# Kernel optimization log

Hardware: AMD Instinct MI355X
Metric: run time of the kernel (lower is better)

Reference implementation:

```python
import jax, jax.numpy as jnp
from jax import lax
import numpy as np

N, C_IN, C_OUT, H, W, D = 16, 32, 64, 128, 128, 5


def setup_inputs() -> dict:
    key = jax.random.key(0)
    k1, k2, k3, k4 = jax.random.split(key, 4)
    x = jax.random.normal(k1, (N, 1, C_IN, H, W), jnp.float32)
    d = jax.random.normal(k2, (N, C_OUT, C_IN, D, D), jnp.float32)
    y = jax.random.normal(k3, (N, C_OUT, 1, H, W), jnp.float32)
    alpha = jax.random.uniform(k4, (N, 1, 1, 1), jnp.float32)
    return {"x": x, "d": d, "y": y, "alpha": alpha, "reg": 1.0}


def _cross_corr(wts, img, pad):
    # out[i, j, u, v] = sum_{h,w} wts[i,h,w] * img[j, h+u-pad, w+v-pad]
    # (valid sums, zero padding). Implements the per-sample full-image conv3d
    # of the torch code (cross-correlation, no kernel flip).
    out = lax.conv_general_dilated(img[:, None], wts[:, None], (1, 1),
                                   [(pad, pad), (pad, pad)])
    return out.transpose(1, 0, 2, 3)  # (Ci_wts, Cj_img, 2*pad+1, 2*pad+1)


def reference(x, d, y, alpha, reg):
    n, _, c_in, h, w = x.shape
    c_out, ds = d.shape[1], d.shape[-1]
    K = c_in * ds * ds
    # Full autocorrelation R[n,c0,c1,a,b] = sum x[c0,h,w]*x[c1,h+a-(ds-1), w+b-(ds-1)]
    R = jax.vmap(lambda xn: _cross_corr(xn, xn, ds - 1))(x[:, 0])  # (n,C,C,2ds-1,2ds-1)
    # Toeplitz block assembly: Q[(c0,p,q),(c1,s,t)] = R[c0,c1, s-p+ds-1, t-q+ds-1]
    shift = jnp.arange(ds)[None, :] - jnp.arange(ds)[:, None] + (ds - 1)  # [p,s]
    Qa = R[:, :, :, shift, :]            # (n,c0,c1,p,s,2ds-1)
    Qb = Qa[..., shift]                  # (n,c0,c1,p,s,q,t)
    Q = Qb.transpose(0, 1, 3, 5, 2, 4, 6).reshape(n, K, K)
    # X^T y: S[n,o,c,u,v] = sum y[o,h,w]*x[c, h+u-p0, w+v-p0], p0=(ds-1)//2
    S = jax.vmap(lambda yn, xn: _cross_corr(yn, xn, (ds - 1) // 2))(y[:, :, 0], x[:, 0])
    P = S.transpose(0, 2, 3, 4, 1).reshape(n, K, c_out)
    # Tikhonov regularization around previous dictionary d
    a = alpha.reshape(n, 1) * (h * w * reg / (ds * ds * c_in))  # (n,1)
    Q = Q + a[:, :, None] * jnp.eye(K, dtype=Q.dtype)
    P = P + a[:, :, None] * d.reshape(n, c_out, K).transpose(0, 2, 1)
    # Batched Cholesky solve: D = Q^{-1} P
    L = jnp.linalg.cholesky(Q)
    z = lax.linalg.triangular_solve(L, P, left_side=True, lower=True)
    Dsol = lax.linalg.triangular_solve(L, z, left_side=True, lower=True, transpose_a=True)
    return Dsol.reshape(n, c_in, ds, ds, c_out).transpose(0, 4, 1, 2, 3)
```

## Files before the change

kernel.cpp:

```cpp
#include <hip/hip_runtime.h>

#define R_SZ    737280
#define Q_SZ    10240000
#define P_SZ    819200
#define LI_SZ   1024000
#define W_SZ    4608000

typedef unsigned short u16;
typedef __attribute__((ext_vector_type(8))) short bf16x8;
typedef __attribute__((ext_vector_type(4))) float f32x4;

#define MFMA16(a, b, c) __builtin_amdgcn_mfma_f32_16x16x32_bf16(a, b, c, 0, 0, 0)

__device__ __forceinline__ float alpha_scale(const float* alpha, const float* reg, int n) {
  return alpha[n] * (16384.0f * reg[0] / 800.0f);
}

__device__ __forceinline__ u16 f2bf(float f) {
  union { float f; unsigned u; } v; v.f = f;
  unsigned r = v.u + 0x7FFFu + ((v.u >> 16) & 1u);
  return (u16)(r >> 16);
}
__device__ __forceinline__ float bf2f(u16 h) {
  union { unsigned u; float f; } v; v.u = ((unsigned)h) << 16; return v.f;
}

__device__ __forceinline__ bf16x8 load8(const u16* p) {
  union { uint4 d; bf16x8 v; } u;
  u.d = *(const uint4*)p;
  return u.v;
}

__device__ __forceinline__ bf16x8 build_frag(const unsigned* w, int s) {
  union { unsigned u[4]; bf16x8 v; } f;
  int b = s >> 1;
  if (s & 1) {
    #pragma unroll
    for (int k = 0; k < 4; ++k) f.u[k] = (w[b + k] >> 16) | (w[b + k + 1] << 16);
  } else {
    #pragma unroll
    for (int k = 0; k < 4; ++k) f.u[k] = w[b + k];
  }
  return f.v;
}

__device__ __forceinline__ void stage_row(u16* slot, int partStride,
                                          const float* __restrict__ img,
                                          int C, int r, bool valid,
                                          int tid, int nthr) {
  for (int idx = tid; idx < C * 16; idx += nthr) {
    int c = idx >> 4, m = idx & 15;
    float v[8];
    if (valid) {
      const float* p = img + ((size_t)c * 128 + r) * 128 + m * 8;
      float4 a = *(const float4*)p;
      float4 b = *(const float4*)(p + 4);
      v[0]=a.x; v[1]=a.y; v[2]=a.z; v[3]=a.w; v[4]=b.x; v[5]=b.y; v[6]=b.z; v[7]=b.w;
    } else {
      #pragma unroll
      for (int k = 0; k < 8; ++k) v[k] = 0.0f;
    }
    union { u16 s[8]; uint2 d[2]; } hh, ll;
    #pragma unroll
    for (int k = 0; k < 8; ++k) {
      u16 h = f2bf(v[k]);
      hh.s[k] = h;
      ll.s[k] = f2bf(v[k] - bf2f(h));
    }
    u16* dh = slot + c * 136 + 4 + m * 8;
    *(uint2*)(dh)     = hh.d[0];
    *(uint2*)(dh + 4) = hh.d[1];
    u16* dl = dh + partStride;
    *(uint2*)(dl)     = ll.d[0];
    *(uint2*)(dl + 4) = ll.d[1];
  }
}

#define SLOT_US 8704
#define PSTR_32 4352
#define YPSTR   8704

__global__ __launch_bounds__(640) void k_corrR_mfma(const float* __restrict__ x,
                                                    float* __restrict__ Rpart) {
  __shared__ __align__(16) u16 lds[5 * SLOT_US];
  int n  = blockIdx.x >> 4;
  int r0 = (blockIdx.x & 15) << 3;
  int tid = threadIdx.x;
  const float* xn = x + (size_t)n * 32 * 128 * 128;

  if (tid < 320) {
    int s = tid / 64, p = (tid >> 5) & 1, c = tid & 31;
    u16* b = lds + s * SLOT_US + p * PSTR_32 + c * 136;
    uint2 z; z.x = 0; z.y = 0;
    *(uint2*)b = z;
    *(uint2*)(b + 132) = z;
  }
  for (int rr = 0; rr < 5; ++rr) {
    int r = r0 + rr;
    stage_row(lds + (r % 5) * SLOT_US, PSTR_32, xn, 32, r, r < 128, tid, 640);
  }

  int wave = tid >> 6, lane = tid & 63;
  int du = wave >> 1, nt = wave & 1;
  int lm = lane & 15, q = lane >> 4;

  f32x4 acc[9][2];
  #pragma unroll
  for (int dvi = 0; dvi < 9; ++dvi)
    #pragma unroll
    for (int mt = 0; mt < 2; ++mt) acc[dvi][mt] = (f32x4){0.f, 0.f, 0.f, 0.f};

  for (int i = r0; i < r0 + 8; ++i) {
    __syncthreads();
    const u16* A  = lds + (i % 5) * SLOT_US;
    const u16* Bp = lds + ((i + du) % 5) * SLOT_US;
    #pragma unroll
    for (int ks = 0; ks < 4; ++ks) {
      int kb = ks * 32 + q * 8;
      bf16x8 af[2][2];
      #pragma unroll
      for (int pa = 0; pa < 2; ++pa)
        #pragma unroll
        for (int mt = 0; mt < 2; ++mt)
          af[pa][mt] = load8(A + pa * PSTR_32 + (mt * 16 + lm) * 136 + 4 + kb);
      #pragma unroll
      for (int pb = 0; pb < 2; ++pb) {
        const u16* wp = Bp + pb * PSTR_32 + (nt * 16 + lm) * 136 + kb;
        uint4 w0 = *(const uint4*)wp;
        uint4 w1 = *(const uint4*)(wp + 8);
        unsigned w[8] = {w0.x, w0.y, w0.z, w0.w, w1.x, w1.y, w1.z, w1.w};
        #pragma unroll
        for (int dvi = 0; dvi < 9; ++dvi) {
          bf16x8 bf = build_frag(w, dvi);
          #pragma unroll
          for (int mt = 0; mt < 2; ++mt)
            #pragma unroll
            for (int pa = 0; pa < 2; ++pa) {
              if (pa == 1 && pb == 1) continue;
              acc[dvi][mt] = MFMA16(af[pa][mt], bf, acc[dvi][mt]);
            }
        }
      }
    }
    __syncthreads();
    if (i + 1 < r0 + 8) {
      int r = i + 5;
      stage_row(lds + (r % 5) * SLOT_US, PSTR_32, xn, 32, r, r < 128, tid, 640);
    }
  }

  float* Rp = Rpart + (size_t)blockIdx.x * 46080;
  #pragma unroll
  for (int dvi = 0; dvi < 9; ++dvi)
    #pragma unroll
    for (int mt = 0; mt < 2; ++mt) {
      float* dst = Rp + (du * 9 + dvi) * 1024 + (nt * 16 + lm) * 32 + mt * 16 + q * 4;
      *(f32x4*)dst = acc[dvi][mt];
    }
}

__global__ void k_reduceR(const float* __restrict__ part, float* __restrict__ R) {
  int idx = blockIdx.x * 256 + threadIdx.x;
  int n = idx / 46080, rem = idx % 46080;
  const float* p = part + (size_t)n * 16 * 46080 + rem;
  float s = 0.0f;
  #pragma unroll
  for (int c = 0; c < 16; ++c) s += p[(size_t)c * 46080];
  R[idx] = s;
}

__global__ __launch_bounds__(640) void k_corrP_mfma(const float* __restrict__ x,
                                                    const float* __restrict__ y,
                                                    float* __restrict__ Ppart) {
  __shared__ __align__(16) u16 xs[5 * SLOT_US];
  __shared__ __align__(16) u16 ys[2 * YPSTR];
  int n  = blockIdx.x >> 4;
  int r0 = (blockIdx.x & 15) << 3;
  int tid = threadIdx.x;
  const float* xn = x + (size_t)n * 32 * 128 * 128;
  const float* yn = y + (size_t)n * 64 * 128 * 128;

  if (tid < 320) {
    int s = tid / 64, p = (tid >> 5) & 1, c = tid & 31;
    u16* b = xs + s * SLOT_US + p * PSTR_32 + c * 136;
    uint2 z; z.x = 0; z.y = 0;
    *(uint2*)b = z;
    *(uint2*)(b + 132) = z;
  }
  for (int rr = -2; rr <= 2; ++rr) {
    int r = r0 + rr;
    stage_row(xs + ((r + 10) % 5) * SLOT_US, PSTR_32, xn, 32, r,
              (r >= 0 && r < 128), tid, 640);
  }
  stage_row(ys, YPSTR, yn, 64, r0, true, tid, 640);

  int wave = tid >> 6, lane = tid & 63;
  int du = (wave >> 1) - 2, mh = wave & 1;
  int lm = lane & 15, q = lane >> 4;

  f32x4 acc[5][2][2];
  #pragma unroll
  for (int dvi = 0; dvi < 5; ++dvi)
    #pragma unroll
    for (int mt = 0; mt < 2; ++mt)
      #pragma unroll
      for (int nt = 0; nt < 2; ++nt)
        acc[dvi][mt][nt] = (f32x4){0.f, 0.f, 0.f, 0.f};

  for (int i = r0; i < r0 + 8; ++i) {
    __syncthreads();
    const u16* Bp = xs + ((i + du + 10) % 5) * SLOT_US;
    #pragma unroll
    for (int ks = 0; ks < 4; ++ks) {
      int kb = ks * 32 + q * 8;
      bf16x8 af[2][2];
      #pragma unroll
      for (int pa = 0; pa < 2; ++pa)
        #pragma unroll
        for (int mt = 0; mt < 2; ++mt)
          af[pa][mt] = load8(ys + pa * YPSTR + (mh * 32 + mt * 16 + lm) * 136 + 4 + kb);
      #pragma unroll
      for (int nt = 0; nt < 2; ++nt)
        #pragma unroll
        for (int pb = 0; pb < 2; ++pb) {
          const u16* wp = Bp + pb * PSTR_32 + (nt * 16 + lm) * 136 + kb;
          uint4 w0 = *(const uint4*)wp;
          uint4 w1 = *(const uint4*)(wp + 8);
          unsigned w[8] = {w0.x, w0.y, w0.z, w0.w, w1.x, w1.y, w1.z, w1.w};
          #pragma unroll
          for (int dvi = 0; dvi < 5; ++dvi) {
            bf16x8 bf = build_frag(w, dvi + 2);
            #pragma unroll
            for (int mt = 0; mt < 2; ++mt)
              #pragma unroll
              for (int pa = 0; pa < 2; ++pa) {
                if (pa == 1 && pb == 1) continue;
                acc[dvi][mt][nt] = MFMA16(af[pa][mt], bf, acc[dvi][mt][nt]);
              }
          }
        }
    }
    __syncthreads();
    if (i + 1 < r0 + 8) {
      int r = i + 3;
      stage_row(xs + ((r + 10) % 5) * SLOT_US, PSTR_32, xn, 32, r,
                (r >= 0 && r < 128), tid, 640);
      stage_row(ys, YPSTR, yn, 64, i + 1, true, tid, 640);
    }
  }

  float* Pp = Ppart + (size_t)blockIdx.x * 51200;
  #pragma unroll
  for (int dvi = 0; dvi < 5; ++dvi)
    #pragma unroll
    for (int mt = 0; mt < 2; ++mt)
      #pragma unroll
      for (int nt = 0; nt < 2; ++nt) {
        float* dst = Pp + ((du + 2) * 5 + dvi) * 2048 + (nt * 16 + lm) * 64
                        + mh * 32 + mt * 16 + q * 4;
        *(f32x4*)dst = acc[dvi][mt][nt];
      }
}

__global__ void k_reduceP(const float* __restrict__ part, const float* __restrict__ d,
                          const float* __restrict__ alpha, const float* __restrict__ reg,
                          float* __restrict__ P) {
  int idx = blockIdx.x * 256 + threadIdx.x;
  int n = idx / 51200, rem = idx % 51200;
  int k = rem >> 6, co = rem & 63;
  int ci = k / 25, ae = k % 25;
  const float* p = part + (size_t)n * 16 * 51200 + (ae * 32 + ci) * 64 + co;
  float s = 0.0f;
  #pragma unroll
  for (int c = 0; c < 16; ++c) s += p[(size_t)c * 51200];
  float a = alpha_scale(alpha, reg, n);
  P[idx] = s + a * d[((size_t)n * 64 + co) * 800 + k];
}

__global__ void k_buildQ(const float* __restrict__ R, float* __restrict__ Q,
                         const float* __restrict__ alpha, const float* __restrict__ reg) {
  int bid = blockIdx.x;
  int n = bid / 800, k1 = bid % 800;
  int c1 = k1 / 25, r1 = k1 % 25, a = r1 / 5, e = r1 % 5;
  float av = alpha_scale(alpha, reg, n);
  const float* Rn = R + (size_t)n * 45 * 1024;
  float* Qrow = Q + ((size_t)n * 800 + k1) * 800;
  for (int k2 = threadIdx.x; k2 < 800; k2 += 256) {
    int c2 = k2 / 25, r2 = k2 % 25, b = r2 / 5, f = r2 % 5;
    int du = b - a, dv = f - e;
    float v = (du >= 0)
      ? Rn[(du * 9 + dv + 4) * 1024 + c2 * 32 + c1]
      : Rn[((-du) * 9 + 4 - dv) * 1024 + c1 * 32 + c2];
    if (k2 == k1) v += av;
    Qrow[k2] = v;
  }
}

#define DS 82

__device__ void diag_factor_invert2(float* As, float* Bs,
                                    float* __restrict__ Ln, float* __restrict__ LnT,
                                    int tid) {
  __shared__ float Dinv_s[16 * 25];
  for (int s = 0; s < 16; ++s) {
    int b = 5 * s;
    float a[5][5], dinv[5];
    #pragma unroll
    for (int ii = 0; ii < 5; ++ii)
      #pragma unroll
      for (int kk = 0; kk <= ii; ++kk) a[ii][kk] = As[(b+ii)*DS + b+kk];
    #pragma unroll
    for (int jj = 0; jj < 5; ++jj) {
      float dd = sqrtf(a[jj][jj]);
      a[jj][jj] = dd; dinv[jj] = 1.0f / dd;
      #pragma unroll
      for (int ii = jj+1; ii < 5; ++ii) a[ii][jj] *= dinv[jj];
      #pragma unroll
      for (int ii = jj+1; ii < 5; ++ii)
        #pragma unroll
        for (int kk = jj+1; kk <= ii; ++kk) a[ii][kk] -= a[ii][jj] * a[kk][jj];
    }
    if (tid < 25) {
      int ii = tid / 5, kk = tid % 5;
      if (kk <= ii) As[(b+ii)*DS + b+kk] = a[ii][kk];
    }
    int m = 75 - b;
    for (int r = tid; r < m; r += 256) {
      int row = b + 5 + r;
      float w[5];
      #pragma unroll
      for (int c = 0; c < 5; ++c) {
        float av2 = As[row*DS + b + c];
        #pragma unroll
        for (int kk = 0; kk < c; ++kk) av2 -= w[kk] * a[c][kk];
        w[c] = av2 * dinv[c];
      }
      #pragma unroll
      for (int c = 0; c < 5; ++c) As[row*DS + b + c] = w[c];
    }
    __syncthreads();
    for (int idx = tid; idx < m*m; idx += 256) {
      int ii = idx / m, kk = idx % m;
      if (kk <= ii) {
        int ri = b+5+ii, rk = b+5+kk;
        float acc2 = As[ri*DS + rk];
        #pragma unroll
        for (int c = 0; c < 5; ++c) acc2 -= As[ri*DS + b+c] * As[rk*DS + b+c];
        As[ri*DS + rk] = acc2;
      }
    }
    __syncthreads();
  }

  if (tid < 16) {
    int i = tid;
    const float* Ab = As + (5*i)*DS + 5*i;
    float L5[5][5], Di[5][5];
    #pragma unroll
    for (int r = 0; r < 5; ++r)
      #pragma unroll
      for (int c = 0; c <= r; ++c) L5[r][c] = Ab[r*DS + c];
    #pragma unroll
    for (int c = 0; c < 5; ++c) {
      #pragma unroll
      for (int r = 0; r < c; ++r) Di[r][c] = 0.0f;
      Di[c][c] = 1.0f / L5[c][c];
      #pragma unroll
      for (int r = c+1; r < 5; ++r) {
        float sacc = 0.0f;
        #pragma unroll
        for (int k = c; k < r; ++k) sacc += L5[r][k] * Di[k][c];
        Di[r][c] = -sacc * (1.0f / L5[r][r]);
      }
    }
    #pragma unroll
    for (int r = 0; r < 5; ++r)
      #pragma unroll
      for (int c = 0; c < 5; ++c) Dinv_s[i*25 + r*5 + c] = Di[r][c];
  }
  __syncthreads();

  if (tid < 80) {
    int j = tid;
    for (int i = 0; i < 16; ++i) {
      float bv[5];
      #pragma unroll
      for (int r = 0; r < 5; ++r) bv[r] = (5*i + r == j) ? 1.0f : 0.0f;
      const float* Arow = As + (5*i)*DS;
      #pragma unroll 5
      for (int k = 0; k < 5*i; ++k) {
        float xc = Bs[k*DS + j];
        #pragma unroll
        for (int r = 0; r < 5; ++r) bv[r] -= Arow[r*DS + k] * xc;
      }
      #pragma unroll
      for (int r = 0; r < 5; ++r) {
        float v = 0.0f;
        #pragma unroll
        for (int c = 0; c <= r; ++c) v += Dinv_s[i*25 + r*5 + c] * bv[c];
        Bs[(5*i + r)*DS + j] = v;
      }
    }
  }
  __syncthreads();
  for (int idx = tid; idx < 6400; idx += 256) {
    int r = idx / 80, c = idx % 80;
    float v = (r >= c) ? Bs[r*DS + c] : 0.0f;
    Ln[idx] = v;
    LnT[c*80 + r] = v;
  }
}

__global__ __launch_bounds__(256) void k_diag0(const float* __restrict__ Q,
                                               float* __restrict__ Linv,
                                               float* __restrict__ LinvT) {
  __shared__ float As[80*DS];
  __shared__ float Bs[80*DS];
  int n = blockIdx.x, tid = threadIdx.x;
  const float* Qn = Q + (size_t)n * 640000;
  for (int idx = tid; idx < 6400; idx += 256) {
    int r = idx / 80, c = idx % 80;
    As[r*DS + c] = Qn[r*800 + c];
  }
  __syncthreads();
  diag_factor_invert2(As, Bs, Linv + (size_t)n*10*6400, LinvT + (size_t)n*10*6400, tid);
}

__global__ __launch_bounds__(256) void k_chol_step(float* __restrict__ Q,
                                                   float* __restrict__ Linv,
                                                   float* __restrict__ LinvT,
                                                   float* __restrict__ Wrm,
                                                   float* __restrict__ Wcm,
                                                   int t) {
  int nt = 9 - t;
  int T = nt * (nt + 1) / 2;
  int n = blockIdx.x / T;
  int rr = blockIdx.x % T;
  int i = 0;
  while (rr >= i + 1) { rr -= i + 1; ++i; }
  int j = rr;
  int bi = t + 1 + i, bj = t + 1 + j;

  __shared__ float Ls[80*DS];
  __shared__ float Aa[80*DS];
  __shared__ float W1[80*DS];
  __shared__ float W2[80*DS];
  int tid = threadIdx.x, tc = tid & 15, tr = tid >> 4;
  float* Qn = Q + (size_t)n * 640000;
  const float* Ln = Linv + ((size_t)n*10 + t) * 6400;

  for (int idx = tid; idx < 6400; idx += 256) {
    int r = idx / 80, c = idx % 80;
    Ls[r*DS + c] = Ln[idx];
    Aa[r*DS + c] = Qn[(size_t)(80*bi + r)*800 + 80*t + c];
  }
  __syncthreads();

  float acc[5][5];
  #pragma unroll
  for (int a = 0; a < 5; ++a)
    #pragma unroll
    for (int b = 0; b < 5; ++b) acc[a][b] = 0.0f;
  for (int k = 0; k < 80; ++k) {
    float av[5], bv[5];
    #pragma unroll
    for (int dd = 0; dd < 5; ++dd) { av[dd] = Aa[(5*tr+dd)*DS + k]; bv[dd] = Ls[(5*tc+dd)*DS + k]; }
    #pragma unroll
    for (int a = 0; a < 5; ++a)
      #pragma unroll
      for (int b = 0; b < 5; ++b) acc[a][b] += av[a] * bv[b];
  }
  #pragma unroll
  for (int a = 0; a < 5; ++a)
    #pragma unroll
    for (int b = 0; b < 5; ++b) W1[(5*tr+a)*DS + 5*tc+b] = acc[a][b];
  if (i == j) {
    int p = t*9 - t*(t-1)/2 + i;
    size_t base = ((size_t)n*45 + p) * 6400;
    #pragma unroll
    for (int a = 0; a < 5; ++a)
      #pragma unroll
      for (int b = 0; b < 5; ++b) {
        Wrm[base + (5*tr+a)*80 + 5*tc+b] = acc[a][b];
        Wcm[base + (5*tc+b)*80 + 5*tr+a] = acc[a][b];
      }
  }
  __syncthreads();

  const float* Wia = W1;
  const float* Wjb = W1;
  if (i != j) {
    for (int idx = tid; idx < 6400; idx += 256) {
      int r = idx / 80, c = idx % 80;
      Aa[r*DS + c] = Qn[(size_t)(80*bj + r)*800 + 80*t + c];
    }
    __syncthreads();
    #pragma unroll
    for (int a = 0; a < 5; ++a)
      #pragma unroll
      for (int b = 0; b < 5; ++b) acc[a][b] = 0.0f;
    for (int k = 0; k < 80; ++k) {
      float av[5], bv[5];
      #pragma unroll
      for (int dd = 0; dd < 5; ++dd) { av[dd] = Aa[(5*tr+dd)*DS + k]; bv[dd] = Ls[(5*tc+dd)*DS + k]; }
      #pragma unroll
      for (int a = 0; a < 5; ++a)
        #pragma unroll
        for (int b = 0; b < 5; ++b) acc[a][b] += av[a] * bv[b];
    }
    #pragma unroll
    for (int a = 0; a < 5; ++a)
      #pragma unroll
      for (int b = 0; b < 5; ++b) W2[(5*tr+a)*DS + 5*tc+b] = acc[a][b];
    Wjb = W2;
    __syncthreads();
  }

  for (int idx = tid; idx < 6400; idx += 256) {
    int r = idx / 80, c = idx % 80;
    Aa[r*DS + c] = Qn[(size_t)(80*bi + r)*800 + 80*bj + c];
  }
  __syncthreads();

  #pragma unroll
  for (int a = 0; a < 5; ++a)
    #pragma unroll
    for (int b = 0; b < 5; ++b) acc[a][b] = 0.0f;
  for (int k = 0; k < 80; ++k) {
    float av[5], bv[5];
    #pragma unroll
    for (int dd = 0; dd < 5; ++dd) { av[dd] = Wia[(5*tr+dd)*DS + k]; bv[dd] = Wjb[(5*tc+dd)*DS + k]; }
    #pragma unroll
    for (int a = 0; a < 5; ++a)
      #pragma unroll
      for (int b = 0; b < 5; ++b) acc[a][b] += av[a] * bv[b];
  }

  bool special = (i == 0 && j == 0);
  if (!special) {
    #pragma unroll
    for (int a = 0; a < 5; ++a)
      #pragma unroll
      for (int b = 0; b < 5; ++b)
        Qn[(size_t)(80*bi + 5*tr+a)*800 + 80*bj + 5*tc+b] =
          Aa[(5*tr+a)*DS + 5*tc+b] - acc[a][b];
  } else {
    #pragma unroll
    for (int a = 0; a < 5; ++a)
      #pragma unroll
      for (int b = 0; b < 5; ++b)
        Aa[(5*tr+a)*DS + 5*tc+b] -= acc[a][b];
    __syncthreads();
    diag_factor_invert2(Aa, Ls,
                        Linv  + ((size_t)n*10 + t + 1) * 6400,
                        LinvT + ((size_t)n*10 + t + 1) * 6400, tid);
  }
}

#define ZS 20

__device__ __forceinline__ void seg80p(const float* __restrict__ Mcur, int i,
                                       const float* __restrict__ Mnext,
                                       float4 (&A)[8],
                                       const float2 (&zc)[80],
                                       float& a0, float& a1) {
  const float* Ci = Mcur + i * 80;
  const float* Ni = Mnext + i * 80;
  #pragma unroll
  for (int h = 0; h < 20; ++h) {
    float4 v = A[h & 7];
    if (h < 12)      A[h & 7]  = *(const float4*)(Ci + 4 * (h + 8));
    else if (h < 16) A[h - 8]  = *(const float4*)(Ni + 4 * (h - 8));
    else             A[h - 16] = *(const float4*)(Ni + 4 * (h - 16));
    a0 += v.x * zc[4*h].x;     a1 += v.x * zc[4*h].y;
    a0 += v.y * zc[4*h + 1].x; a1 += v.y * zc[4*h + 1].y;
    a0 += v.z * zc[4*h + 2].x; a1 += v.z * zc[4*h + 2].y;
    a0 += v.w * zc[4*h + 3].x; a1 += v.w * zc[4*h + 3].y;
  }
}

__global__ __launch_bounds__(160, 1) void k_solve(const float* __restrict__ Linv,
                                                  const float* __restrict__ LinvT,
                                                  const float* __restrict__ Wrm,
                                                  const float* __restrict__ Wcm,
                                                  const float* __restrict__ P,
                                                  float* __restrict__ out) {
  __shared__ __align__(16) float z2[2 * 800 * 2];
  int n   = blockIdx.x >> 4;
  int qg4 = (blockIdx.x & 15) << 2;
  int tid = threadIdx.x;
  int i   = tid % 80;
  int cp  = tid / 80;
  const float* Lb  = Linv  + (size_t)n * 10 * 6400;
  const float* LTb = LinvT + (size_t)n * 10 * 6400;
  const float* Wr  = Wrm + (size_t)n * 45 * 6400;
  const float* Wc  = Wcm + (size_t)n * 45 * 6400;

  for (int idx = tid; idx < 3200; idx += 160) {
    int k = idx >> 2, cc = idx & 3;
    z2[((cc >> 1) * 800 + k) * 2 + (cc & 1)] =
        P[((size_t)n * 800 + k) * 64 + qg4 + cc];
  }

  float2 zc[80];
  float4 A[8];
  {
    const float* Mi = Lb + i * 80;
    #pragma unroll
    for (int q = 0; q < 8; ++q) A[q] = *(const float4*)(Mi + 4 * q);
  }

  for (int t = 0; t < 10; ++t) {
    __syncthreads();
    int zb = (cp * 800 + 80 * t) * 2;
    #pragma unroll
    for (int m = 0; m < 40; ++m) {
      float4 v = *(const float4*)&z2[zb + 4 * m];
      zc[2*m]     = make_float2(v.x, v.y);
      zc[2*m + 1] = make_float2(v.z, v.w);
    }
    int nseg = 9 - t;
    const float* Mc = Wr + (size_t)(t * 9 - t * (t - 1) / 2) * 6400;
    const float* nxt = (nseg > 0) ? Mc
                      : (t < 9 ? Lb + (t + 1) * 6400 : LTb + 9 * 6400);
    float a0 = 0.f, a1 = 0.f;
    seg80p(Lb + t * 6400, i, nxt, A, zc, a0, a1);
    __syncthreads();
    *(float2*)&z2[(cp * 800 + 80 * t + i) * 2] = make_float2(a0, a1);
    __syncthreads();
    #pragma unroll
    for (int m = 0; m < 40; ++m) {
      float4 v = *(const float4*)&z2[zb + 4 * m];
      zc[2*m]     = make_float2(v.x, v.y);
      zc[2*m + 1] = make_float2(v.z, v.w);
    }
    for (int s = 0; s < nseg; ++s) {
      const float* nx2 = (s + 1 < nseg) ? Mc + (size_t)(s + 1) * 6400
                                        : Lb + (t + 1) * 6400;
      float b0 = 0.f, b1 = 0.f;
      seg80p(Mc + (size_t)s * 6400, i, nx2, A, zc, b0, b1);
      float2* zp = (float2*)&z2[(cp * 800 + 80 * (t + 1 + s) + i) * 2];
      float2 v = *zp; v.x -= b0; v.y -= b1; *zp = v;
    }
  }

  for (int t = 9; t >= 0; --t) {
    __syncthreads();
    int zb = (cp * 800 + 80 * t) * 2;
    #pragma unroll
    for (int m = 0; m < 40; ++m) {
      float4 v = *(const float4*)&z2[zb + 4 * m];
      zc[2*m]     = make_float2(v.x, v.y);
      zc[2*m + 1] = make_float2(v.z, v.w);
    }
    const float* nxt;
    if (t > 0) {
      int p0 = (t - 1) * 9 - (t - 1) * (t - 2) / 2;
      nxt = Wc + (size_t)p0 * 6400;
    } else nxt = Lb;
    float a0 = 0.f, a1 = 0.f;
    seg80p(LTb + t * 6400, i, nxt, A, zc, a0, a1);
    __syncthreads();
    *(float2*)&z2[(cp * 800 + 80 * t + i) * 2] = make_float2(a0, a1);
    __syncthreads();
    #pragma unroll
    for (int m = 0; m < 40; ++m) {
      float4 v = *(const float4*)&z2[zb + 4 * m];
      zc[2*m]     = make_float2(v.x, v.y);
      zc[2*m + 1] = make_float2(v.z, v.w);
    }
    for (int u = t - 1; u >= 0; --u) {
      int p = u * 9 - u * (u - 1) / 2 + (t - u - 1);
      const float* nx2;
      if (u > 0) {
        int pn = (u - 1) * 9 - (u - 1) * (u - 2) / 2 + (t - u);
        nx2 = Wc + (size_t)pn * 6400;
      } else nx2 = (t > 0) ? LTb + (t - 1) * 6400 : Lb;
      float b0 = 0.f, b1 = 0.f;
      seg80p(Wc + (size_t)p * 6400, i, nx2, A, zc, b0, b1);
      float2* zp = (float2*)&z2[(cp * 800 + 80 * u + i) * 2];
      float2 v = *zp; v.x -= b0; v.y -= b1; *zp = v;
    }
  }

  __syncthreads();
  for (int idx = tid; idx < 3200; idx += 160) {
    int c = idx / 800, k = idx % 800;
    out[((size_t)n * 64 + qg4 + c) * 800 + k] =
        z2[((c >> 1) * 800 + k) * 2 + (c & 1)];
  }
}

extern "C" void kernel_launch(void* const* d_in, const int* in_sizes, int n_in,
                              void* d_out, int out_size, void* d_ws, size_t ws_size,
                              hipStream_t stream) {
  const float* x     = (const float*)d_in[0];
  const float* d     = (const float*)d_in[1];
  const float* y     = (const float*)d_in[2];
  const float* alpha = (const float*)d_in[3];
  const float* reg   = (const float*)d_in[4];
  float* out = (float*)d_out;
  float* ws  = (float*)d_ws;

  float* R    = ws;
  float* Q    = R + R_SZ;
  float* P    = Q + Q_SZ;
  float* Li   = P + P_SZ;
  float* part = Li + LI_SZ;
  float* LiT  = part;
  float* Wrm  = part + LI_SZ;
  float* Wcm  = Wrm + W_SZ;

  k_corrR_mfma<<<256, 640, 0, stream>>>(x, part);
  k_reduceR<<<R_SZ / 256, 256, 0, stream>>>(part, R);
  k_corrP_mfma<<<256, 640, 0, stream>>>(x, y, part);
  k_reduceP<<<P_SZ / 256, 256, 0, stream>>>(part, d, alpha, reg, P);
  k_buildQ<<<16 * 800, 256, 0, stream>>>(R, Q, alpha, reg);

  k_diag0<<<16, 256, 0, stream>>>(Q, Li, LiT);
  for (int t = 0; t < 9; ++t) {
    int nt = 9 - t;
    k_chol_step<<<16 * nt * (nt + 1) / 2, 256, 0, stream>>>(Q, Li, LiT, Wrm, Wcm, t);
  }

  k_solve<<<16 * 16, 160, 0, stream>>>(Li, LiT, Wrm, Wcm, P, out);
}
```

Before: 1.409 ms.

## Split Cholesky step into panel and trailing-update kernels to avoid redundant panel GEMMs

Each blocked Cholesky step used to recompute the panel products W = A·Linv^T inside every trailing-update block, up to twice per block. The step is now two kernels: one computes each panel block once and writes it to global memory, and the trailing kernel reads the precomputed W tiles and does only the rank update. This cuts redundant FLOPs and shared-memory use per block. The cost is one extra launch per step (nine in total) and a global round-trip for W.

```diff
diff --git a/kernel.cpp b/kernel.cpp
--- a/kernel.cpp
+++ b/kernel.cpp
@@ -426,12 +426,60 @@
   diag_factor_invert2(As, Bs, Linv + (size_t)n*10*6400, LinvT + (size_t)n*10*6400, tid);
 }
 
-__global__ __launch_bounds__(256) void k_chol_step(float* __restrict__ Q,
-                                                   float* __restrict__ Linv,
-                                                   float* __restrict__ LinvT,
-                                                   float* __restrict__ Wrm,
-                                                   float* __restrict__ Wcm,
-                                                   int t) {
+__global__ __launch_bounds__(256) void k_panel(const float* __restrict__ Q,
+                                               const float* __restrict__ Linv,
+                                               float* __restrict__ Wrm,
+                                               float* __restrict__ Wcm,
+                                               int t) {
+  int nt = 9 - t;
+  int n = blockIdx.x / nt;
+  int s = blockIdx.x % nt;
+  int bu = t + 1 + s;
+
+  __shared__ float Ls[80*DS];
+  __shared__ float Aa[80*DS];
+  int tid = threadIdx.x, tc = tid & 15, tr = tid >> 4;
+  const float* Qn = Q + (size_t)n * 640000;
+  const float* Ln = Linv + ((size_t)n*10 + t) * 6400;
+
+  for (int idx = tid; idx < 6400; idx += 256) {
+    int r = idx / 80, c = idx % 80;
+    Ls[r*DS + c] = Ln[idx];
+    Aa[r*DS + c] = Qn[(size_t)(80*bu + r)*800 + 80*t + c];
+  }
+  __syncthreads();
+
+  float acc[5][5];
+  #pragma unroll
+  for (int a = 0; a < 5; ++a)
+    #pragma unroll
+    for (int b = 0; b < 5; ++b) acc[a][b] = 0.0f;
+  for (int k = 0; k < 80; ++k) {
+    float av[5], bv[5];
+    #pragma unroll
+    for (int dd = 0; dd < 5; ++dd) { av[dd] = Aa[(5*tr+dd)*DS + k]; bv[dd] = Ls[(5*tc+dd)*DS + k]; }
+    #pragma unroll
+    for (int a = 0; a < 5; ++a)
+      #pragma unroll
+      for (int b = 0; b < 5; ++b) acc[a][b] += av[a] * bv[b];
+  }
+
+  int p = t*9 - t*(t-1)/2 + s;
+  size_t base = ((size_t)n*45 + p) * 6400;
+  #pragma unroll
+  for (int a = 0; a < 5; ++a)
+    #pragma unroll
+    for (int b = 0; b < 5; ++b) {
+      Wrm[base + (5*tr+a)*80 + 5*tc+b] = acc[a][b];
+      Wcm[base + (5*tc+b)*80 + 5*tr+a] = acc[a][b];
+    }
+}
+
+__global__ __launch_bounds__(256) void k_trail(float* __restrict__ Q,
+                                               float* __restrict__ Linv,
+                                               float* __restrict__ LinvT,
+                                               const float* __restrict__ Wrm,
+                                               int t) {
   int nt = 9 - t;
   int T = nt * (nt + 1) / 2;
   int n = blockIdx.x / T;
@@ -441,21 +489,29 @@
   int j = rr;
   int bi = t + 1 + i, bj = t + 1 + j;
 
-  __shared__ float Ls[80*DS];
-  __shared__ float Aa[80*DS];
-  __shared__ float W1[80*DS];
-  __shared__ float W2[80*DS];
+  __shared__ float Wi[80*DS];
+  __shared__ float Wj[80*DS];
+  __shared__ float As[80*DS];
   int tid = threadIdx.x, tc = tid & 15, tr = tid >> 4;
   float* Qn = Q + (size_t)n * 640000;
-  const float* Ln = Linv + ((size_t)n*10 + t) * 6400;
+  int pb = t*9 - t*(t-1)/2;
+  const float* Wri = Wrm + ((size_t)n*45 + pb + i) * 6400;
+  const float* Wrj = Wrm + ((size_t)n*45 + pb + j) * 6400;
 
   for (int idx = tid; idx < 6400; idx += 256) {
     int r = idx / 80, c = idx % 80;
-    Ls[r*DS + c] = Ln[idx];
-    Aa[r*DS + c] = Qn[(size_t)(80*bi + r)*800 + 80*t + c];
+    Wi[r*DS + c] = Wri[idx];
+    As[r*DS + c] = Qn[(size_t)(80*bi + r)*800 + 80*bj + c];
+  }
+  if (i != j) {
+    for (int idx = tid; idx < 6400; idx += 256) {
+      int r = idx / 80, c = idx % 80;
+      Wj[r*DS + c] = Wrj[idx];
+    }
   }
   __syncthreads();
 
+  const float* Wjb = (i != j) ? Wj : Wi;
   float acc[5][5];
   #pragma unroll
   for (int a = 0; a < 5; ++a)
@@ -464,72 +520,7 @@
   for (int k = 0; k < 80; ++k) {
     float av[5], bv[5];
     #pragma unroll
-    for (int dd = 0; dd < 5; ++dd) { av[dd] = Aa[(5*tr+dd)*DS + k]; bv[dd] = Ls[(5*tc+dd)*DS + k]; }
-    #pragma unroll
-    for (int a = 0; a < 5; ++a)
-      #pragma unroll
-      for (int b = 0; b < 5; ++b) acc[a][b] += av[a] * bv[b];
-  }
-  #pragma unroll
-  for (int a = 0; a < 5; ++a)
-    #pragma unroll
-    for (int b = 0; b < 5; ++b) W1[(5*tr+a)*DS + 5*tc+b] = acc[a][b];
-  if (i == j) {
-    int p = t*9 - t*(t-1)/2 + i;
-    size_t base = ((size_t)n*45 + p) * 6400;
-    #pragma unroll
-    for (int a = 0; a < 5; ++a)
-      #pragma unroll
-      for (int b = 0; b < 5; ++b) {
-        Wrm[base + (5*tr+a)*80 + 5*tc+b] = acc[a][b];
-        Wcm[base + (5*tc+b)*80 + 5*tr+a] = acc[a][b];
-      }
-  }
-  __syncthreads();
-
-  const float* Wia = W1;
-  const float* Wjb = W1;
-  if (i != j) {
-    for (int idx = tid; idx < 6400; idx += 256) {
-      int r = idx / 80, c = idx % 80;
-      Aa[r*DS + c] = Qn[(size_t)(80*bj + r)*800 + 80*t + c];
-    }
-    __syncthreads();
-    #pragma unroll
-    for (int a = 0; a < 5; ++a)
-      #pragma unroll
-      for (int b = 0; b < 5; ++b) acc[a][b] = 0.0f;
-    for (int k = 0; k < 80; ++k) {
-      float av[5], bv[5];
-      #pragma unroll
-      for (int dd = 0; dd < 5; ++dd) { av[dd] = Aa[(5*tr+dd)*DS + k]; bv[dd] = Ls[(5*tc+dd)*DS + k]; }
-      #pragma unroll
-      for (int a = 0; a < 5; ++a)
-        #pragma unroll
-        for (int b = 0; b < 5; ++b) acc[a][b] += av[a] * bv[b];
-    }
-    #pragma unroll
-    for (int a = 0; a < 5; ++a)
-      #pragma unroll
-      for (int b = 0; b < 5; ++b) W2[(5*tr+a)*DS + 5*tc+b] = acc[a][b];
-    Wjb = W2;
-    __syncthreads();
-  }
-
-  for (int idx = tid; idx < 6400; idx += 256) {
-    int r = idx / 80, c = idx % 80;
-    Aa[r*DS + c] = Qn[(size_t)(80*bi + r)*800 + 80*bj + c];
-  }
-  __syncthreads();
-
-  #pragma unroll
-  for (int a = 0; a < 5; ++a)
-    #pragma unroll
-    for (int b = 0; b < 5; ++b) acc[a][b] = 0.0f;
-  for (int k = 0; k < 80; ++k) {
-    float av[5], bv[5];
-    #pragma unroll
-    for (int dd = 0; dd < 5; ++dd) { av[dd] = Wia[(5*tr+dd)*DS + k]; bv[dd] = Wjb[(5*tc+dd)*DS + k]; }
+    for (int dd = 0; dd < 5; ++dd) { av[dd] = Wi[(5*tr+dd)*DS + k]; bv[dd] = Wjb[(5*tc+dd)*DS + k]; }
     #pragma unroll
     for (int a = 0; a < 5; ++a)
       #pragma unroll
@@ -543,15 +534,15 @@
       #pragma unroll
       for (int b = 0; b < 5; ++b)
         Qn[(size_t)(80*bi + 5*tr+a)*800 + 80*bj + 5*tc+b] =
-          Aa[(5*tr+a)*DS + 5*tc+b] - acc[a][b];
+          As[(5*tr+a)*DS + 5*tc+b] - acc[a][b];
   } else {
     #pragma unroll
     for (int a = 0; a < 5; ++a)
       #pragma unroll
       for (int b = 0; b < 5; ++b)
-        Aa[(5*tr+a)*DS + 5*tc+b] -= acc[a][b];
-    __syncthreads();
-    diag_factor_invert2(Aa, Ls,
+        As[(5*tr+a)*DS + 5*tc+b] -= acc[a][b];
+    __syncthreads();
+    diag_factor_invert2(As, Wj,
                         Linv  + ((size_t)n*10 + t + 1) * 6400,
                         LinvT + ((size_t)n*10 + t + 1) * 6400, tid);
   }
@@ -720,7 +711,8 @@
   k_diag0<<<16, 256, 0, stream>>>(Q, Li, LiT);
   for (int t = 0; t < 9; ++t) {
     int nt = 9 - t;
-    k_chol_step<<<16 * nt * (nt + 1) / 2, 256, 0, stream>>>(Q, Li, LiT, Wrm, Wcm, t);
+    k_panel<<<16 * nt, 256, 0, stream>>>(Q, Li, Wrm, Wcm, t);
+    k_trail<<<16 * nt * (nt + 1) / 2, 256, 0, stream>>>(Q, Li, LiT, Wrm, t);
   }
 
   k_solve<<<16 * 16, 160, 0, stream>>>(Li, LiT, Wrm, Wcm, P, out);
```

Result: faster. 1.342 ms (-4.8%).
